# Kernel optimization log

Measured on AMD Instinct MI355X. Metric: run time of the kernel, lower is better.

The kernel has to match this reference:

```python
import jax, jax.numpy as jnp
import numpy as np

KEEP_ATTN = 0.9   # 1 - attn_pdrop
KEEP_RESID = 0.9  # 1 - resid_pdrop
B, T, C, H = 2, 2048, 1024, 16


def setup_inputs() -> dict:
    key = jax.random.key(0)
    ks = jax.random.split(key, 5)
    x = jax.random.normal(ks[0], (B, T, C), jnp.float32)
    Wqkv = jax.random.normal(ks[1], (C, 3 * C), jnp.float32) / np.float32(np.sqrt(C))
    bqkv = jnp.zeros((3 * C,), jnp.float32)
    Wproj = jax.random.normal(ks[2], (C, C), jnp.float32) / np.float32(np.sqrt(C))
    bproj = jnp.zeros((C,), jnp.float32)
    # dropout keep-masks (replace the attn_pdrop_key / resid_pdrop_key args)
    attn_drop_mask = jax.random.bernoulli(ks[3], KEEP_ATTN, (B, H, T, T))
    resid_drop_mask = jax.random.bernoulli(ks[4], KEEP_RESID, (B, T, C))
    return dict(x=x, Wqkv=Wqkv, bqkv=bqkv, Wproj=Wproj, bproj=bproj,
                attn_drop_mask=attn_drop_mask, resid_drop_mask=resid_drop_mask)


def reference(x, Wqkv, bqkv, Wproj, bproj, attn_drop_mask, resid_drop_mask):
    Bx, Tx, Cx = x.shape
    Hh = attn_drop_mask.shape[1]
    hd = Cx // Hh  # head_dim
    qkv = x @ Wqkv + bqkv                              # [B,T,3C]
    q, k, v = jnp.split(qkv, 3, axis=-1)
    q = q.reshape(Bx, Tx, Hh, hd).swapaxes(1, 2)       # [B,H,T,hd]
    k = k.reshape(Bx, Tx, Hh, hd).swapaxes(1, 2)
    v = v.reshape(Bx, Tx, Hh, hd).swapaxes(1, 2)
    attn = jnp.einsum('bhqd,bhkd->bhqk', q, k) / np.float32(np.sqrt(hd))  # [B,H,T,T]
    causal = jnp.tril(jnp.ones((Tx, Tx), dtype=bool))  # lower-triangular bias
    attn = jnp.where(causal, attn, -jnp.inf)
    attn = jax.nn.softmax(attn, axis=-1)
    attn = jnp.where(attn_drop_mask, attn / np.float32(KEEP_ATTN), 0.0)
    y = jnp.einsum('bhqk,bhkd->bhqd', attn, v)         # [B,H,T,hd]
    y = y.swapaxes(1, 2).reshape(Bx, Tx, Cx)           # [B,T,C]
    y = y @ Wproj + bproj
    y = jnp.where(resid_drop_mask, y / np.float32(KEEP_RESID), 0.0)
    return y
```

## Files before the change

kernel.cpp:

```cpp
#include <hip/hip_runtime.h>
#include <cstdint>
#include <cstddef>

typedef unsigned int u32;
typedef unsigned short u16;
typedef short s8v __attribute__((ext_vector_type(8)));
typedef __bf16 bf8v __attribute__((ext_vector_type(8)));
typedef float f4v __attribute__((ext_vector_type(4)));

#define B_ 2
#define T_ 2048
#define C_ 1024
#define H_ 16
#define HD 64
#define LOG2E 1.4426950408889634f
#define SCL (0.125f * LOG2E)

__device__ __forceinline__ u16 f2bf(float f){
  u32 u = __builtin_bit_cast(u32, f);
  u += 0x7fffu + ((u >> 16) & 1u);
  return (u16)(u >> 16);
}

__device__ __forceinline__ f4v mfma16(s8v a, s8v b, f4v c){
  return __builtin_amdgcn_mfma_f32_16x16x32_bf16((bf8v)a, (bf8v)b, c, 0, 0, 0);
}

__device__ __forceinline__ void gload_lds16(const void* g, void* l){
  __builtin_amdgcn_global_load_lds((const __attribute__((address_space(1))) u32*)g,
                                   (__attribute__((address_space(3))) u32*)l,
                                   16, 0, 0);
}

__global__ __launch_bounds__(256) void cast_bf16_k(const float* __restrict__ in,
                                                   u16* __restrict__ out, int n8){
  int i = blockIdx.x * 256 + threadIdx.x;
  if (i >= n8) return;
  const float4* p = (const float4*)in;
  float4 a = p[i*2], b = p[i*2+1];
  uint4 o = make_uint4(
     (u32)f2bf(a.x) | ((u32)f2bf(a.y) << 16),
     (u32)f2bf(a.z) | ((u32)f2bf(a.w) << 16),
     (u32)f2bf(b.x) | ((u32)f2bf(b.y) << 16),
     (u32)f2bf(b.z) | ((u32)f2bf(b.w) << 16));
  ((uint4*)out)[i] = o;
}

__global__ __launch_bounds__(256) void tcast_k(const float* __restrict__ src,
                                               u16* __restrict__ dst, int R, int C){
  __shared__ u16 tile[64][65];
  int t = threadIdx.x;
  int c0 = blockIdx.x * 64, r0 = blockIdx.y * 64;
  int col = t & 63, rb = t >> 6;
#pragma unroll
  for (int i = 0; i < 16; i++){
    int row = rb + i*4;
    tile[row][col] = f2bf(src[(size_t)(r0+row)*C + (c0+col)]);
  }
  __syncthreads();
#pragma unroll
  for (int i = 0; i < 16; i++){
    int oc = rb + i*4;
    dst[(size_t)(c0+oc)*R + (r0+col)] = tile[col][oc];
  }
}

__global__ __launch_bounds__(256) void tv_k(const u16* __restrict__ qkv,
                                            u16* __restrict__ VT){
  __shared__ u16 tile[64][65];
  int t = threadIdx.x;
  int tt = blockIdx.x, bh = blockIdx.y;
  int b = bh >> 4, h = bh & 15;
  int col = t & 63, rb = t >> 6;
  const u16* src = qkv + (size_t)(b*T_ + tt*64)*(3*C_) + 2*C_ + h*HD;
#pragma unroll
  for (int i = 0; i < 16; i++){
    int row = rb + i*4;
    tile[row][col] = src[(size_t)row*(3*C_) + col];
  }
  __syncthreads();
  u16* dst = VT + (size_t)bh*HD*T_ + tt*64;
#pragma unroll
  for (int i = 0; i < 16; i++){
    int d = rb + i*4;
    dst[(size_t)d*T_ + col] = tile[col][d];
  }
}

template<int MODE>
__global__ __launch_bounds__(256) void gemm_k(const u16* __restrict__ A,
                        const u16* __restrict__ Bt,
                        const float* __restrict__ bias, void* __restrict__ outp,
                        const int* __restrict__ rmask,
                        int M, int N, int K){
  __shared__ __align__(16) u16 As[128*32];
  __shared__ __align__(16) u16 Bs[128*32];
  int t = threadIdx.x;
  int w = t >> 6, l = t & 63;
  int lo = l & 15, lg = l >> 4;
  int m0 = blockIdx.x * 128, n0 = blockIdx.y * 128;
  int wm = (w >> 1) * 64, wn = (w & 1) * 64;

  f4v acc[4][4];
#pragma unroll
  for (int i=0;i<4;i++)
#pragma unroll
    for (int j=0;j<4;j++) acc[i][j] = (f4v){0.f,0.f,0.f,0.f};

  for (int ks = 0; ks < K; ks += 32){
#pragma unroll
    for (int i = 0; i < 2; i++){
      int c = t + i*256;
      int row = c >> 2, k8 = (c & 3) * 8;
      gload_lds16(A  + (size_t)(m0+row)*K + ks + k8, (char*)As + (size_t)(w*64 + i*256)*16);
      gload_lds16(Bt + (size_t)(n0+row)*K + ks + k8, (char*)Bs + (size_t)(w*64 + i*256)*16);
    }
    __syncthreads();
    s8v af[4], bfr[4];
#pragma unroll
    for (int mt=0; mt<4; mt++)
      af[mt]  = *(const s8v*)(As + (wm + mt*16 + lo)*32 + lg*8);
#pragma unroll
    for (int nt=0; nt<4; nt++)
      bfr[nt] = *(const s8v*)(Bs + (wn + nt*16 + lo)*32 + lg*8);
#pragma unroll
    for (int mt=0; mt<4; mt++)
#pragma unroll
      for (int nt=0; nt<4; nt++)
        acc[mt][nt] = mfma16(af[mt], bfr[nt], acc[mt][nt]);
    __syncthreads();
  }

#pragma unroll
  for (int mt=0; mt<4; mt++){
#pragma unroll
    for (int nt=0; nt<4; nt++){
#pragma unroll
      for (int r=0; r<4; r++){
        int row = m0 + wm + mt*16 + lg*4 + r;
        int col = n0 + wn + nt*16 + lo;
        float v = acc[mt][nt][r] + bias[col];
        if (MODE == 0){
          ((u16*)outp)[(size_t)row*N + col] = f2bf(v);
        } else {
          float o = rmask[(size_t)row*N + col] ? v * (1.0f/0.9f) : 0.0f;
          ((float*)outp)[(size_t)row*N + col] = o;
        }
      }
    }
  }
}

__global__ __launch_bounds__(256, 4) void attn_k(const u16* __restrict__ qkv,
                        const u16* __restrict__ VT,
                        const int* __restrict__ amask,
                        u16* __restrict__ Y){
  __shared__ __align__(16) u16 Ks[2][64*64];
  __shared__ __align__(16) u16 Vs[2][64*64];
  __shared__ __align__(16) u16 Ps[4][16*64];
  const int t = threadIdx.x;
  const int w = t >> 6, l = t & 63;
  const int lo = l & 15, lg = l >> 4;

  const int n = blockIdx.x;
  const int bh = n & 31;
  const int j = n >> 5, a = j & 7, bb = j >> 3;
  const int qt = (bb & 1) ? (31 - a - 8*(bb >> 1)) : (a + 8*(bb >> 1));
  const int b = bh >> 4, h = bh & 15;
  const int q0 = qt * 64;
  const int qmaxw = q0 + w*16 + 15;

  const u16* Kg = qkv + (size_t)(b*T_)*(3*C_) + C_ + h*HD;
  const u16* Vg = VT + (size_t)bh*HD*T_;
  const int* mg = amask + (size_t)bh*T_*T_ + (size_t)(q0 + w*16)*T_;

  int qrow = q0 + w*16 + lo;
  const u16* qp = qkv + (size_t)(b*T_ + qrow)*(3*C_) + h*HD;
  s8v qf0 = *(const s8v*)(qp + lg*8);
  s8v qf1 = *(const s8v*)(qp + 32 + lg*8);

  f4v acc[4];
#pragma unroll
  for (int i=0;i<4;i++) acc[i] = (f4v){0.f,0.f,0.f,0.f};
  float mrow[4], lsum[4];
#pragma unroll
  for (int r=0;r<4;r++){ mrow[r] = -1e30f; lsum[r] = 0.f; }

  auto STAGE = [&](int buf, int kt){
#pragma unroll
    for (int i = 0; i < 2; i++){
      int c = t + i*256;
      int row = c >> 3;
      int cc = (c & 7) ^ (row & 7);
      gload_lds16(Kg + (size_t)(kt*64 + row)*(3*C_) + cc*8,
                  (char*)Ks[buf] + (size_t)(w*64 + i*256)*16);
      gload_lds16(Vg + (size_t)row*T_ + kt*64 + cc*8,
                  (char*)Vs[buf] + (size_t)(w*64 + i*256)*16);
    }
  };

  auto MLOAD = [&](int kt, int* m){
#pragma unroll
    for (int k4 = 0; k4 < 4; k4++)
#pragma unroll
      for (int r = 0; r < 4; r++)
        m[k4*4 + r] = mg[(size_t)(lg*4 + r)*T_ + kt*64 + k4*16 + lo];
  };

  auto TILE = [&](int kt, int cur, const int* m, bool diag){
    const char* kb = (const char*)Ks[cur];
    const char* vb = (const char*)Vs[cur];
    float p[16];
    float nm[4];
#pragma unroll
    for (int r=0;r<4;r++) nm[r] = mrow[r];
#pragma unroll
    for (int k4 = 0; k4 < 4; k4++){
      bool active = !diag || (kt*64 + k4*16 <= qmaxw);
      f4v s = (f4v){0.f,0.f,0.f,0.f};
      if (active){
#pragma unroll
        for (int kk = 0; kk < 2; kk++){
          int krow = k4*16 + lo;
          int off = krow*128 + (((kk*4 + lg) ^ (krow & 7)) << 4);
          s8v kf = *(const s8v*)(kb + off);
          s = mfma16(kk ? qf1 : qf0, kf, s);
        }
      }
#pragma unroll
      for (int r=0;r<4;r++){
        float sv = active ? s[r] : -1e30f;
        if (diag){
          int kidx = kt*64 + k4*16 + lo;
          int qi = q0 + w*16 + lg*4 + r;
          sv = (kidx <= qi) ? sv : -1e30f;
        }
        p[k4*4 + r] = sv;
        nm[r] = fmaxf(nm[r], sv);
      }
    }
#pragma unroll
    for (int r=0;r<4;r++){
      float v = nm[r];
      v = fmaxf(v, __shfl_xor(v, 1));
      v = fmaxf(v, __shfl_xor(v, 2));
      v = fmaxf(v, __shfl_xor(v, 4));
      v = fmaxf(v, __shfl_xor(v, 8));
      nm[r] = v;
    }
    bool grow = false;
#pragma unroll
    for (int r=0;r<4;r++) grow = grow || (nm[r] > mrow[r] + 8.0f);
    if (__any(grow)){
#pragma unroll
      for (int r=0;r<4;r++){
        float f = exp2f((mrow[r] - nm[r]) * SCL);
        lsum[r] *= f;
#pragma unroll
        for (int d=0; d<4; d++) acc[d][r] *= f;
        mrow[r] = nm[r];
      }
    }
    float rs[4] = {0.f,0.f,0.f,0.f};
    char* pw = (char*)&Ps[w][0];
#pragma unroll
    for (int k4=0;k4<4;k4++){
#pragma unroll
      for (int r=0;r<4;r++){
        float e = exp2f((p[k4*4 + r] - mrow[r]) * SCL);
        rs[r] += e;
        u16 pb = m[k4*4 + r] ? f2bf(e) : (u16)0;
        int prow = lg*4 + r;
        int off = (prow*128 + (k4*16 + lo)*2) ^ ((prow & 7) << 4);
        *(u16*)(pw + off) = pb;
      }
    }
#pragma unroll
    for (int r=0;r<4;r++){
      float v = rs[r];
      v += __shfl_xor(v, 1);
      v += __shfl_xor(v, 2);
      v += __shfl_xor(v, 4);
      v += __shfl_xor(v, 8);
      lsum[r] += v;
    }
    s8v pf[2];
#pragma unroll
    for (int kk=0;kk<2;kk++){
      int off = lo*128 + (((kk*4 + lg) ^ (lo & 7)) << 4);
      pf[kk] = *(const s8v*)(pw + off);
    }
#pragma unroll
    for (int dt=0; dt<4; dt++){
#pragma unroll
      for (int kk=0; kk<2; kk++){
        int vrow = dt*16 + lo;
        int voff = vrow*128 + (((kk*4 + lg) ^ (vrow & 7)) << 4);
        s8v vf = *(const s8v*)(vb + voff);
        acc[dt] = mfma16(pf[kk], vf, acc[dt]);
      }
    }
  };

  int mcur[16], mnext[16];
  STAGE(0, 0);
  MLOAD(0, mcur);
  __syncthreads();

  int cur = 0;
  for (int kt = 0; kt < qt; kt++){
    STAGE(cur ^ 1, kt + 1);
    MLOAD(kt + 1, mnext);
    TILE(kt, cur, mcur, false);
    __syncthreads();
#pragma unroll
    for (int i=0;i<16;i++) mcur[i] = mnext[i];
    cur ^= 1;
  }
  TILE(qt, cur, mcur, true);

#pragma unroll
  for (int r=0;r<4;r++){
    int qi = q0 + w*16 + lg*4 + r;
    float inv = 1.0f / (lsum[r] * 0.9f);
    u16* yp = Y + (size_t)(b*T_ + qi)*C_ + h*HD;
#pragma unroll
    for (int dt=0; dt<4; dt++){
      yp[dt*16 + lo] = f2bf(acc[dt][r] * inv);
    }
  }
}

extern "C" void kernel_launch(void* const* d_in, const int* in_sizes, int n_in,
                              void* d_out, int out_size, void* d_ws, size_t ws_size,
                              hipStream_t stream){
  const float* x     = (const float*)d_in[0];
  const float* Wqkv  = (const float*)d_in[1];
  const float* bqkv  = (const float*)d_in[2];
  const float* Wproj = (const float*)d_in[3];
  const float* bproj = (const float*)d_in[4];
  const int* amask = (const int*)d_in[5];
  const int* rmask = (const int*)d_in[6];
  float* out = (float*)d_out;

  char* ws = (char*)d_ws;
  u16* xb     = (u16*)(ws);
  u16* WqkvT  = (u16*)(ws + (size_t)( 8<<20));
  u16* WprojT = (u16*)(ws + (size_t)(14<<20));
  u16* qkv    = (u16*)(ws + (size_t)(16<<20));
  u16* VT     = (u16*)(ws + (size_t)(40<<20));
  u16* Yb     = (u16*)(ws + (size_t)(48<<20));

  cast_bf16_k<<<dim3(2048), dim3(256), 0, stream>>>(x, xb, (B_*T_*C_)/8);
  tcast_k<<<dim3(48, 16), dim3(256), 0, stream>>>(Wqkv, WqkvT, C_, 3*C_);
  tcast_k<<<dim3(16, 16), dim3(256), 0, stream>>>(Wproj, WprojT, C_, C_);
  gemm_k<0><<<dim3(32, 24), dim3(256), 0, stream>>>(xb, WqkvT, bqkv, qkv, nullptr,
                                                    B_*T_, 3*C_, C_);
  tv_k<<<dim3(32, 32), dim3(256), 0, stream>>>(qkv, VT);
  attn_k<<<dim3(1024), dim3(256), 0, stream>>>(qkv, VT, amask, Yb);
  gemm_k<1><<<dim3(32, 8), dim3(256), 0, stream>>>(Yb, WprojT, bproj, out, rmask,
                                                   B_*T_, C_, C_);
}
```

Before: 804.7 us.

## Bit-pack attention dropout mask, double-buffer GEMM LDS, add MFMA priority hints

A new pre-pass kernel reads the int32 attention dropout mask once, only the causal part, and packs it into 64-bit ballot words. The attention kernel then reads one u64 per row per key tile instead of sixteen scattered int loads per lane. The GEMM kernel gains double-buffered LDS staging so the next K-slice loads while the current one computes, and s_setprio hints bracket the MFMA sections in attention. The extra pack kernel still reads the full causal mask, but it does so with coalesced loads and shrinks what the attention loop has to fetch.

```diff
diff --git a/kernel.cpp b/kernel.cpp
--- a/kernel.cpp
+++ b/kernel.cpp
@@ -4,6 +4,7 @@
 
 typedef unsigned int u32;
 typedef unsigned short u16;
+typedef unsigned long long u64;
 typedef short s8v __attribute__((ext_vector_type(8)));
 typedef __bf16 bf8v __attribute__((ext_vector_type(8)));
 typedef float f4v __attribute__((ext_vector_type(4)));
@@ -30,6 +31,20 @@
   __builtin_amdgcn_global_load_lds((const __attribute__((address_space(1))) u32*)g,
                                    (__attribute__((address_space(3))) u32*)l,
                                    16, 0, 0);
+}
+
+__global__ __launch_bounds__(256) void pack_k(const int* __restrict__ am,
+                                              u64* __restrict__ pm){
+  int gw = (blockIdx.x * 256 + threadIdx.x) >> 6;
+  int l = threadIdx.x & 63;
+  int bh = gw >> 11, q = gw & 2047;
+  const int* src = am + (size_t)bh*T_*T_ + (size_t)q*T_;
+  u64* dst = pm + ((size_t)bh*T_ + q)*(T_/64);
+  int nc = (q >> 6) + 1;
+  for (int c = 0; c < nc; c++){
+    u64 bits = __ballot(src[c*64 + l] != 0);
+    if (l == 0) dst[c] = bits;
+  }
 }
 
 __global__ __launch_bounds__(256) void cast_bf16_k(const float* __restrict__ in,
@@ -93,42 +108,51 @@
                         const float* __restrict__ bias, void* __restrict__ outp,
                         const int* __restrict__ rmask,
                         int M, int N, int K){
-  __shared__ __align__(16) u16 As[128*32];
-  __shared__ __align__(16) u16 Bs[128*32];
+  __shared__ __align__(16) u16 As[2][128*32];
+  __shared__ __align__(16) u16 Bs[2][128*32];
   int t = threadIdx.x;
   int w = t >> 6, l = t & 63;
   int lo = l & 15, lg = l >> 4;
   int m0 = blockIdx.x * 128, n0 = blockIdx.y * 128;
   int wm = (w >> 1) * 64, wn = (w & 1) * 64;
 
-  f4v acc[4][4];
-#pragma unroll
-  for (int i=0;i<4;i++)
-#pragma unroll
-    for (int j=0;j<4;j++) acc[i][j] = (f4v){0.f,0.f,0.f,0.f};
-
-  for (int ks = 0; ks < K; ks += 32){
+  auto STAGE = [&](int buf, int ks){
 #pragma unroll
     for (int i = 0; i < 2; i++){
       int c = t + i*256;
       int row = c >> 2, k8 = (c & 3) * 8;
-      gload_lds16(A  + (size_t)(m0+row)*K + ks + k8, (char*)As + (size_t)(w*64 + i*256)*16);
-      gload_lds16(Bt + (size_t)(n0+row)*K + ks + k8, (char*)Bs + (size_t)(w*64 + i*256)*16);
-    }
-    __syncthreads();
+      gload_lds16(A  + (size_t)(m0+row)*K + ks + k8,
+                  (char*)As[buf] + (size_t)(w*64 + i*256)*16);
+      gload_lds16(Bt + (size_t)(n0+row)*K + ks + k8,
+                  (char*)Bs[buf] + (size_t)(w*64 + i*256)*16);
+    }
+  };
+
+  f4v acc[4][4];
+#pragma unroll
+  for (int i=0;i<4;i++)
+#pragma unroll
+    for (int j=0;j<4;j++) acc[i][j] = (f4v){0.f,0.f,0.f,0.f};
+
+  STAGE(0, 0);
+  __syncthreads();
+  int cur = 0;
+  for (int ks = 0; ks < K; ks += 32){
+    if (ks + 32 < K) STAGE(cur ^ 1, ks + 32);
     s8v af[4], bfr[4];
 #pragma unroll
     for (int mt=0; mt<4; mt++)
-      af[mt]  = *(const s8v*)(As + (wm + mt*16 + lo)*32 + lg*8);
+      af[mt]  = *(const s8v*)(&As[cur][0] + (wm + mt*16 + lo)*32 + lg*8);
 #pragma unroll
     for (int nt=0; nt<4; nt++)
-      bfr[nt] = *(const s8v*)(Bs + (wn + nt*16 + lo)*32 + lg*8);
+      bfr[nt] = *(const s8v*)(&Bs[cur][0] + (wn + nt*16 + lo)*32 + lg*8);
 #pragma unroll
     for (int mt=0; mt<4; mt++)
 #pragma unroll
       for (int nt=0; nt<4; nt++)
         acc[mt][nt] = mfma16(af[mt], bfr[nt], acc[mt][nt]);
     __syncthreads();
+    cur ^= 1;
   }
 
 #pragma unroll
@@ -153,7 +177,7 @@
 
 __global__ __launch_bounds__(256, 4) void attn_k(const u16* __restrict__ qkv,
                         const u16* __restrict__ VT,
-                        const int* __restrict__ amask,
+                        const u64* __restrict__ pmask,
                         u16* __restrict__ Y){
   __shared__ __align__(16) u16 Ks[2][64*64];
   __shared__ __align__(16) u16 Vs[2][64*64];
@@ -172,7 +196,7 @@
 
   const u16* Kg = qkv + (size_t)(b*T_)*(3*C_) + C_ + h*HD;
   const u16* Vg = VT + (size_t)bh*HD*T_;
-  const int* mg = amask + (size_t)bh*T_*T_ + (size_t)(q0 + w*16)*T_;
+  const u64* pmw = pmask + ((size_t)bh*T_ + q0 + w*16)*(T_/64);
 
   int qrow = q0 + w*16 + lo;
   const u16* qp = qkv + (size_t)(b*T_ + qrow)*(3*C_) + h*HD;
@@ -199,21 +223,18 @@
     }
   };
 
-  auto MLOAD = [&](int kt, int* m){
-#pragma unroll
-    for (int k4 = 0; k4 < 4; k4++)
-#pragma unroll
-      for (int r = 0; r < 4; r++)
-        m[k4*4 + r] = mg[(size_t)(lg*4 + r)*T_ + kt*64 + k4*16 + lo];
-  };
-
-  auto TILE = [&](int kt, int cur, const int* m, bool diag){
+  auto TILE = [&](int kt, int cur, bool diag){
     const char* kb = (const char*)Ks[cur];
     const char* vb = (const char*)Vs[cur];
+    u64 pb[4];
+#pragma unroll
+    for (int r=0;r<4;r++) pb[r] = pmw[(size_t)(lg*4 + r)*(T_/64) + kt];
+
     float p[16];
     float nm[4];
 #pragma unroll
     for (int r=0;r<4;r++) nm[r] = mrow[r];
+    __builtin_amdgcn_s_setprio(1);
 #pragma unroll
     for (int k4 = 0; k4 < 4; k4++){
       bool active = !diag || (kt*64 + k4*16 <= qmaxw);
@@ -239,6 +260,7 @@
         nm[r] = fmaxf(nm[r], sv);
       }
     }
+    __builtin_amdgcn_s_setprio(0);
 #pragma unroll
     for (int r=0;r<4;r++){
       float v = nm[r];
@@ -269,10 +291,10 @@
       for (int r=0;r<4;r++){
         float e = exp2f((p[k4*4 + r] - mrow[r]) * SCL);
         rs[r] += e;
-        u16 pb = m[k4*4 + r] ? f2bf(e) : (u16)0;
+        u16 pv = ((pb[r] >> (k4*16 + lo)) & 1ull) ? f2bf(e) : (u16)0;
         int prow = lg*4 + r;
         int off = (prow*128 + (k4*16 + lo)*2) ^ ((prow & 7) << 4);
-        *(u16*)(pw + off) = pb;
+        *(u16*)(pw + off) = pv;
       }
     }
 #pragma unroll
@@ -290,6 +312,7 @@
       int off = lo*128 + (((kk*4 + lg) ^ (lo & 7)) << 4);
       pf[kk] = *(const s8v*)(pw + off);
     }
+    __builtin_amdgcn_s_setprio(1);
 #pragma unroll
     for (int dt=0; dt<4; dt++){
 #pragma unroll
@@ -300,24 +323,20 @@
         acc[dt] = mfma16(pf[kk], vf, acc[dt]);
       }
     }
+    __builtin_amdgcn_s_setprio(0);
   };
 
-  int mcur[16], mnext[16];
   STAGE(0, 0);
-  MLOAD(0, mcur);
   __syncthreads();
 
   int cur = 0;
   for (int kt = 0; kt < qt; kt++){
     STAGE(cur ^ 1, kt + 1);
-    MLOAD(kt + 1, mnext);
-    TILE(kt, cur, mcur, false);
+    TILE(kt, cur, false);
     __syncthreads();
-#pragma unroll
-    for (int i=0;i<16;i++) mcur[i] = mnext[i];
     cur ^= 1;
   }
-  TILE(qt, cur, mcur, true);
+  TILE(qt, cur, true);
 
 #pragma unroll
   for (int r=0;r<4;r++){
@@ -350,14 +369,16 @@
   u16* qkv    = (u16*)(ws + (size_t)(16<<20));
   u16* VT     = (u16*)(ws + (size_t)(40<<20));
   u16* Yb     = (u16*)(ws + (size_t)(48<<20));
-
+  u64* pm     = (u64*)(ws + (size_t)(56<<20));
+
+  pack_k<<<dim3(16384), dim3(256), 0, stream>>>(amask, pm);
   cast_bf16_k<<<dim3(2048), dim3(256), 0, stream>>>(x, xb, (B_*T_*C_)/8);
   tcast_k<<<dim3(48, 16), dim3(256), 0, stream>>>(Wqkv, WqkvT, C_, 3*C_);
   tcast_k<<<dim3(16, 16), dim3(256), 0, stream>>>(Wproj, WprojT, C_, C_);
   gemm_k<0><<<dim3(32, 24), dim3(256), 0, stream>>>(xb, WqkvT, bqkv, qkv, nullptr,
                                                     B_*T_, 3*C_, C_);
   tv_k<<<dim3(32, 32), dim3(256), 0, stream>>>(qkv, VT);
-  attn_k<<<dim3(1024), dim3(256), 0, stream>>>(qkv, VT, amask, Yb);
+  attn_k<<<dim3(1024), dim3(256), 0, stream>>>(qkv, VT, pm, Yb);
   gemm_k<1><<<dim3(32, 8), dim3(256), 0, stream>>>(Yb, WprojT, bproj, out, rmask,
                                                    B_*T_, C_, C_);
 }
```

After: 864.2 us. +7.4%, slower.
